# Kernel tuning notes

Hardware: AMD Instinct MI355X
Metric: run time of the kernel (lower is better)

Reference implementation:

```python
import jax, jax.numpy as jnp
import numpy as np

B, L, K, G, C, S = 1024, 32, 8, 8, 128, 32
D_IN = 2 * L + K + S  # masked z (L) + mask (L) + target (K) + shared (S)
TAU = 1.0
EPS = 1e-5
NEG_INF = -1e9  # stands in for torch's -9e15 diagonal fill; sigmoid(-1e9)=0


def setup_inputs() -> dict:
    key = jax.random.key(0)
    ks = jax.random.split(key, 24)
    eye = jnp.eye(K, dtype=bool)
    kaiming = lambda k, shape: jax.random.uniform(k, shape, jnp.float32, -1.0, 1.0) * np.sqrt(6.0 / shape[-1])
    return {
        "z_sample": jax.random.normal(ks[0], (B, L), jnp.float32),
        "target": jax.random.randint(ks[1], (B,), 0, K),
        "z_mean": jax.random.normal(ks[2], (B, L), jnp.float32),
        "z_logstd": 0.1 * jax.random.normal(ks[3], (B, L), jnp.float32),
        "z_shared": jax.random.normal(ks[4], (B, S), jnp.float32),
        "u_gumbel": jax.random.uniform(ks[5], (B, L, K), jnp.float32),
        "u_adj": jax.random.uniform(ks[6], (B, G, K, K), jnp.float32),
        "target_params": 0.1 * jax.random.normal(ks[7], (L, K), jnp.float32),
        "enco_theta": jnp.where(eye, NEG_INF, jax.random.normal(ks[8], (K, K), jnp.float32)),
        "enco_gamma": jnp.where(eye, NEG_INF, jax.random.normal(ks[9], (K, K), jnp.float32)),
        "W1": kaiming(ks[10], (L, C, D_IN)),
        "b1": jnp.zeros((L, C), jnp.float32),
        "gn1_w": jnp.ones((L, C), jnp.float32),
        "gn1_b": jnp.zeros((L, C), jnp.float32),
        "W2": kaiming(ks[11], (L, C, C)),
        "b2": jnp.zeros((L, C), jnp.float32),
        "gn2_w": jnp.ones((L, C), jnp.float32),
        "gn2_b": jnp.zeros((L, C), jnp.float32),
        "W3": 0.01 * jax.random.normal(ks[12], (L, 2, C), jnp.float32),
        "b3": jnp.zeros((L, 2), jnp.float32),
        "tanh_scale": jnp.zeros((L, 2), jnp.float32),
    }


def _mv_linear(x, W, b):
    # x: [B,G,L,d_in], W: [L,d_out,d_in] -> [B,G,L,d_out]  (per-latent independent linear)
    return jnp.einsum("bgld,lhd->bglh", x, W) + b


def _mv_groupnorm(x, w, b):
    # GroupNorm(L groups over L*C channels) == per-(sample, latent) normalization over C
    mu = x.mean(-1, keepdims=True)
    var = ((x - mu) ** 2).mean(-1, keepdims=True)
    return (x - mu) * jax.lax.rsqrt(var + EPS) * w + b


def reference(z_sample, target, z_mean, z_logstd, z_shared, u_gumbel, u_adj,
              target_params, enco_theta, enco_gamma,
              W1, b1, gn1_w, gn1_b, W2, b2, gn2_w, gn2_b, W3, b3, tanh_scale):
    dt = z_sample.dtype
    target_oh = jax.nn.one_hot(target, K, dtype=dt)  # [B,K]

    # hard gumbel-softmax with straight-through estimator: psi assigns latents to causal vars
    g = -jnp.log(-jnp.log(u_gumbel + 1e-10) + 1e-10)
    soft = jax.nn.softmax((target_params[None] + g) / TAU, axis=-1)  # [B,L,K]
    hard = jax.nn.one_hot(jnp.argmax(soft, axis=-1), K, dtype=dt)
    psi = hard + soft - jax.lax.stop_gradient(soft)  # [B,L,K]

    # ENCO graph sampling: edge prob = sigmoid(theta)*sigmoid(gamma), Bernoulli samples
    edge_prob = jax.nn.sigmoid(enco_theta) * jax.nn.sigmoid(enco_gamma)  # [K,K]
    adj = (u_adj < edge_prob[None, None]).astype(dt)  # [B,G,K,K], adj[k,l]=1: k->l

    # latent-level parent mask: mask[b,g,i,j]=1 iff latent j is a parent of latent i
    latent_mask = jnp.einsum("bil,bgkl,bjk->bgij", psi, adj, psi)  # [B,G,L,L]
    latent_mask = latent_mask * (1.0 - jnp.eye(L, dtype=dt))

    # per-latent network input: [masked parents, mask, intervention indicator, shared]
    z_masked = latent_mask * z_sample[:, None, None, :]                        # [B,G,L,L]
    t_inp = jnp.broadcast_to((psi * target_oh[:, None, :])[:, None], (B, G, L, K))
    zs = jnp.broadcast_to(z_shared[:, None, None, :], (B, G, L, S))
    s_inp = jnp.concatenate([z_masked, latent_mask, t_inp, zs], axis=-1)       # [B,G,L,D_IN]

    h = jax.nn.silu(_mv_groupnorm(_mv_linear(s_inp, W1, b1), gn1_w, gn1_b))
    h = jax.nn.silu(_mv_groupnorm(_mv_linear(h, W2, b2), gn2_w, gn2_b))
    h = _mv_linear(h, W3, b3)                                                  # [B,G,L,2]
    sc = jnp.exp(tanh_scale)                                                   # [L,2]
    h = jnp.tanh(h / sc) * sc                                                  # MultivarStableTanh
    prior_mean, prior_logstd = h[..., 0], h[..., 1]                            # [B,G,L]

    # KL(q(z) || p(z)) per latent, averaged over graph samples, summed over latents
    var_q = jnp.exp(2.0 * z_logstd)[:, None]                                   # [B,1,L]
    kld = (prior_logstd - z_logstd[:, None]
           + (var_q + (z_mean[:, None] - prior_mean) ** 2) / (2.0 * jnp.exp(2.0 * prior_logstd))
           - 0.5)                                                              # [B,G,L]
    return kld.mean(axis=1).sum(axis=-1)                                       # [B]
```

## Files before the change

kernel.cpp:

```cpp
#include <hip/hip_runtime.h>
#include <hip/hip_bf16.h>

#define B_DIM 1024
#define L_DIM 32
#define K_DIM 8
#define G_DIM 8
#define C_DIM 128
#define S_DIM 32
#define DIN   104

typedef __bf16  bf16x8 __attribute__((ext_vector_type(8)));
typedef float   f32x4  __attribute__((ext_vector_type(4)));

union frag_u { uint4 u; bf16x8 v; };

static __device__ __forceinline__ unsigned int pk2(float a, float b) {
    __hip_bfloat162 h = __float22bfloat162_rn(make_float2(a, b));
    union { __hip_bfloat162 h; unsigned int u; } v; v.h = h; return v.u;
}
static __device__ __forceinline__ bf16x8 ld_frag(const unsigned short* p) {
    frag_u t; t.u = *(const uint4*)p; return t.v;
}
static __device__ __forceinline__ bf16x8 u2f(uint4 u) {
    frag_u t; t.u = u; return t.v;
}
static __device__ __forceinline__ float siluf(float x) {
    return __fdividef(x, 1.0f + __expf(-x));
}

__global__ __launch_bounds__(256) void prep_kernel(
    const float* __restrict__ u_gumbel,
    const float* __restrict__ u_adj,
    const float* __restrict__ target_params,
    const float* __restrict__ enco_theta,
    const float* __restrict__ enco_gamma,
    const int*   __restrict__ target,
    const float* __restrict__ W1,
    const float* __restrict__ W2,
    float*       __restrict__ out,
    unsigned char* __restrict__ cvarpk,
    unsigned int*  __restrict__ wsmask,
    unsigned short* __restrict__ wscr)
{
    const int t = threadIdx.x;
    if (blockIdx.x >= 1024) {
        int gtid  = (blockIdx.x - 1024) * 256 + t;
        int lane  = gtid & 63;
        int ks    = (gtid >> 6) & 3;
        int mt    = (gtid >> 8) & 3;
        int wm    = (gtid >> 10) & 1;
        int l     = (gtid >> 11) & 31;
        int which = gtid >> 16;
        int m  = 16 * (4 * wm + mt) + (lane & 15);
        int k0 = ks * 32 + (lane >> 4) * 8;
        uint4 o;
        if (which == 0) {
            if (k0 >= 104) {
                o = make_uint4(0u, 0u, 0u, 0u);
            } else {
                const float* p = W1 + (size_t)l * 13312 + m * 104 + k0;
                float4 a = *(const float4*)p, bq = *(const float4*)(p + 4);
                o = make_uint4(pk2(a.x, a.y), pk2(a.z, a.w), pk2(bq.x, bq.y), pk2(bq.z, bq.w));
            }
        } else {
            const float* p = W2 + (size_t)l * 16384 + m * 128 + k0;
            float4 a = *(const float4*)p, bq = *(const float4*)(p + 4);
            o = make_uint4(pk2(a.x, a.y), pk2(a.z, a.w), pk2(bq.x, bq.y), pk2(bq.z, bq.w));
        }
        *(uint4*)(wscr + (size_t)gtid * 8) = o;
        return;
    }

    __shared__ double ep[64];
    __shared__ unsigned char cv8[32];
    __shared__ unsigned long long adjb[8];
    const int b = blockIdx.x;
    if (t < 64) {
        double th = (double)enco_theta[t];
        double ga = (double)enco_gamma[t];
        ep[t] = (1.0 / (1.0 + exp(-th))) * (1.0 / (1.0 + exp(-ga)));
    }
    if (t == 0) out[b] = 0.0f;
    __syncthreads();

    {
        const int l = t >> 3, k = t & 7;
        float uf = u_gumbel[b * 256 + t];
        float gf = -__logf(-__logf(uf + 1e-10f) + 1e-10f);
        float vf = target_params[t] + gf;
        float vm = vf; int bk = k;
        #pragma unroll
        for (int off = 1; off < 8; off <<= 1) {
            float ov = __shfl_xor(vm, off, 64);
            int  obk = __shfl_xor(bk, off, 64);
            if (ov > vm || (ov == vm && obk < bk)) { vm = ov; bk = obk; }
        }
        int amb = ((k != bk) && (vm - vf < 1e-3f)) ? 1 : 0;
        #pragma unroll
        for (int off = 1; off < 8; off <<= 1) amb |= __shfl_xor(amb, off, 64);
        if (amb) {
            double ud = (double)uf;
            double gd = -log(-log(ud + 1e-10) + 1e-10);
            double vd = (double)target_params[t] + gd;
            int bk2 = k;
            #pragma unroll
            for (int off = 1; off < 8; off <<= 1) {
                double ov = __shfl_xor(vd, off, 64);
                int   obk = __shfl_xor(bk2, off, 64);
                if (ov > vd || (ov == vd && obk < bk2)) { vd = ov; bk2 = obk; }
            }
            bk = bk2;
        }
        if (k == 0) {
            int tg = target[b];
            unsigned char pkd = (unsigned char)(bk | ((bk == tg) ? 8 : 0));
            cvarpk[b * 32 + l] = pkd;
            cv8[l] = pkd;
        }
    }
    {
        const int wv = t >> 6, lane = t & 63;
        #pragma unroll
        for (int q = 0; q < 2; ++q) {
            int gg = wv + 4 * q;
            double u = (double)u_adj[b * 512 + gg * 64 + lane];
            unsigned long long m = __ballot(u < ep[lane]);
            if (lane == 0) adjb[gg] = m;
        }
    }
    __syncthreads();

    {
        const int g = t >> 5, l = t & 31;
        int lam = cv8[l] & 7;
        unsigned long long bits = adjb[g] >> lam;
        unsigned int mask = 0u;
        #pragma unroll
        for (int j = 0; j < 32; ++j) {
            int kap = cv8[j] & 7;
            mask |= ((unsigned int)(bits >> (kap * 8)) & 1u) << j;
        }
        mask &= ~(1u << l);
        wsmask[l * 8192 + b * 8 + g] = mask;
    }
}

__global__ __launch_bounds__(256, 3) void fused_kernel(
    const float* __restrict__ z_sample,
    const float* __restrict__ z_mean,
    const float* __restrict__ z_logstd,
    const float* __restrict__ z_shared,
    const float* __restrict__ pb1,
    const float* __restrict__ g1w,
    const float* __restrict__ g1b,
    const float* __restrict__ pb2,
    const float* __restrict__ g2w,
    const float* __restrict__ g2b,
    const float* __restrict__ W3,
    const float* __restrict__ pb3,
    const float* __restrict__ tsc,
    const unsigned short* __restrict__ wscr,
    const unsigned char*  __restrict__ cvarpk,
    const unsigned int*   __restrict__ wsmask,
    float* __restrict__ out)
{
    __shared__ __align__(16) unsigned short XH[4][32][136];
    __shared__ float p_g1w[128], p_g1b[128], p_b1[128];
    __shared__ float p_g2w[128], p_g2b[128], p_b2[128];
    __shared__ float p_w3[2][128];
    __shared__ float p_b3[2], p_ts[2];
    __shared__ unsigned int  msk[128];
    __shared__ unsigned char cvl[16];

    const int tid  = threadIdx.x;
    const int w    = tid >> 6, lane = tid & 63;
    const int lo   = lane & 15, hi = lane >> 4;
    const int l    = blockIdx.x & 31;
    const int grp  = blockIdx.x >> 5;

    if (tid < 128) {
        int c = tid;
        p_g1w[c] = g1w[l * 128 + c];  p_g1b[c] = g1b[l * 128 + c];
        p_b1[c]  = pb1[l * 128 + c];  p_w3[0][c] = W3[l * 256 + c];
        msk[c]   = wsmask[l * 8192 + grp * 128 + c];
    } else {
        int c = tid - 128;
        p_g2w[c] = g2w[l * 128 + c];  p_g2b[c] = g2b[l * 128 + c];
        p_b2[c]  = pb2[l * 128 + c];  p_w3[1][c] = W3[l * 256 + 128 + c];
    }
    if (tid < 16) cvl[tid] = cvarpk[(size_t)(grp * 16 + tid) * 32 + l];
    if (tid == 0) {
        p_b3[0] = pb3[l * 2];  p_b3[1] = pb3[l * 2 + 1];
        p_ts[0] = tsc[l * 2];  p_ts[1] = tsc[l * 2 + 1];
    }
    __syncthreads();

    bf16x8 bq[2][4];
    #pragma unroll
    for (int nt = 0; nt < 2; ++nt) {
        int r  = w * 32 + nt * 16 + lo;
        int bl = r >> 3;
        int bg = grp * 16 + bl;
        unsigned int m32 = msk[r];
        unsigned int mq  = (m32 >> (hi * 8)) & 0xffu;
        const float4* zp = (const float4*)(z_sample + bg * 32 + hi * 8);
        float4 za = zp[0], zb = zp[1];
        uint4 f0;
        f0.x = pk2((mq & 1u)   ? za.x : 0.f, (mq & 2u)   ? za.y : 0.f);
        f0.y = pk2((mq & 4u)   ? za.z : 0.f, (mq & 8u)   ? za.w : 0.f);
        f0.z = pk2((mq & 16u)  ? zb.x : 0.f, (mq & 32u)  ? zb.y : 0.f);
        f0.w = pk2((mq & 64u)  ? zb.z : 0.f, (mq & 128u) ? zb.w : 0.f);
        uint4 f1;
        f1.x = ((mq & 1u)   ? 0x3F80u : 0u) | ((mq & 2u)   ? 0x3F800000u : 0u);
        f1.y = ((mq & 4u)   ? 0x3F80u : 0u) | ((mq & 8u)   ? 0x3F800000u : 0u);
        f1.z = ((mq & 16u)  ? 0x3F80u : 0u) | ((mq & 32u)  ? 0x3F800000u : 0u);
        f1.w = ((mq & 64u)  ? 0x3F80u : 0u) | ((mq & 128u) ? 0x3F800000u : 0u);
        unsigned int cb8 = cvl[bl];
        int lam = cb8 & 7, tf = (cb8 >> 3) & 1;
        int zsb = (hi == 0) ? 24 : (hi - 1) * 8;
        const float4* sp = (const float4*)(z_shared + bg * 32 + zsb);
        float4 sa = sp[0], sb = sp[1];
        uint4 fz;
        fz.x = pk2(sa.x, sa.y); fz.y = pk2(sa.z, sa.w);
        fz.z = pk2(sb.x, sb.y); fz.w = pk2(sb.z, sb.w);
        unsigned int ohw = tf ? (0x3F80u << ((lam & 1) << 4)) : 0u;
        int lq = lam >> 1;
        uint4 fo;
        fo.x = (lq == 0) ? ohw : 0u;
        fo.y = (lq == 1) ? ohw : 0u;
        fo.z = (lq == 2) ? ohw : 0u;
        fo.w = (lq == 3) ? ohw : 0u;
        bool h0 = (hi == 0);
        uint4 f2, f3;
        f2.x = h0 ? fo.x : fz.x;  f2.y = h0 ? fo.y : fz.y;
        f2.z = h0 ? fo.z : fz.z;  f2.w = h0 ? fo.w : fz.w;
        f3.x = h0 ? fz.x : 0u;    f3.y = h0 ? fz.y : 0u;
        f3.z = h0 ? fz.z : 0u;    f3.w = h0 ? fz.w : 0u;
        bq[nt][0] = u2f(f0); bq[nt][1] = u2f(f1);
        bq[nt][2] = u2f(f2); bq[nt][3] = u2f(f3);
    }

    const float inv128 = 1.0f / 128.0f;

    f32x4 acc[8][2];
    #pragma unroll
    for (int cb = 0; cb < 8; ++cb)
        #pragma unroll
        for (int nt = 0; nt < 2; ++nt) acc[cb][nt] = (f32x4){0.f, 0.f, 0.f, 0.f};
    {
        const unsigned short* w1p = wscr + (size_t)(l * 32) * 512 + lane * 8;
        #pragma unroll
        for (int ks = 0; ks < 4; ++ks) {
            #pragma unroll
            for (int half = 0; half < 2; ++half) {
                bf16x8 wf[4];
                #pragma unroll
                for (int q = 0; q < 4; ++q)
                    wf[q] = ld_frag(w1p + ((half * 4 + q) * 4 + ks) * 512);
                #pragma unroll
                for (int q = 0; q < 4; ++q) {
                    int cb = half * 4 + q;
                    acc[cb][0] = __builtin_amdgcn_mfma_f32_16x16x32_bf16(
                        wf[q], bq[0][ks], acc[cb][0], 0, 0, 0);
                    acc[cb][1] = __builtin_amdgcn_mfma_f32_16x16x32_bf16(
                        wf[q], bq[1][ks], acc[cb][1], 0, 0, 0);
                }
            }
        }
    }

    float s1[2] = {0.f, 0.f}, s2[2] = {0.f, 0.f};
    #pragma unroll
    for (int cb = 0; cb < 8; ++cb) {
        float4 b4 = *(const float4*)&p_b1[cb * 16 + hi * 4];
        #pragma unroll
        for (int rg = 0; rg < 4; ++rg) {
            float bias = ((const float*)&b4)[rg];
            #pragma unroll
            for (int nt = 0; nt < 2; ++nt) {
                float v = acc[cb][nt][rg] + bias;
                acc[cb][nt][rg] = v;
                s1[nt] += v;  s2[nt] += v * v;
            }
        }
    }
    float mu[2], rstd[2];
    #pragma unroll
    for (int nt = 0; nt < 2; ++nt) {
        s1[nt] += __shfl_xor(s1[nt], 16, 64);  s1[nt] += __shfl_xor(s1[nt], 32, 64);
        s2[nt] += __shfl_xor(s2[nt], 16, 64);  s2[nt] += __shfl_xor(s2[nt], 32, 64);
        float m_  = s1[nt] * inv128;
        float var = s2[nt] * inv128 - m_ * m_;
        mu[nt] = m_;  rstd[nt] = rsqrtf(var + 1e-5f);
    }
    #pragma unroll
    for (int cb = 0; cb < 8; ++cb) {
        float4 gw4 = *(const float4*)&p_g1w[cb * 16 + hi * 4];
        float4 gb4 = *(const float4*)&p_g1b[cb * 16 + hi * 4];
        #pragma unroll
        for (int nt = 0; nt < 2; ++nt) {
            float sl[4];
            #pragma unroll
            for (int rg = 0; rg < 4; ++rg) {
                float x = (acc[cb][nt][rg] - mu[nt]) * rstd[nt] * ((const float*)&gw4)[rg]
                          + ((const float*)&gb4)[rg];
                sl[rg] = siluf(x);
            }
            *(uint2*)&XH[w][nt * 16 + lo][cb * 16 + hi * 4] =
                make_uint2(pk2(sl[0], sl[1]), pk2(sl[2], sl[3]));
        }
    }

    #pragma unroll
    for (int cb = 0; cb < 8; ++cb)
        #pragma unroll
        for (int nt = 0; nt < 2; ++nt) acc[cb][nt] = (f32x4){0.f, 0.f, 0.f, 0.f};
    {
        const unsigned short* w2p = wscr + (size_t)((32 + l) * 32) * 512 + lane * 8;
        #pragma unroll
        for (int ks = 0; ks < 4; ++ks) {
            bf16x8 bf0 = ld_frag(&XH[w][lo][ks * 32 + hi * 8]);
            bf16x8 bf1 = ld_frag(&XH[w][16 + lo][ks * 32 + hi * 8]);
            #pragma unroll
            for (int half = 0; half < 2; ++half) {
                bf16x8 wf[4];
                #pragma unroll
                for (int q = 0; q < 4; ++q)
                    wf[q] = ld_frag(w2p + ((half * 4 + q) * 4 + ks) * 512);
                #pragma unroll
                for (int q = 0; q < 4; ++q) {
                    int cb = half * 4 + q;
                    acc[cb][0] = __builtin_amdgcn_mfma_f32_16x16x32_bf16(
                        wf[q], bf0, acc[cb][0], 0, 0, 0);
                    acc[cb][1] = __builtin_amdgcn_mfma_f32_16x16x32_bf16(
                        wf[q], bf1, acc[cb][1], 0, 0, 0);
                }
            }
        }
    }

    float t1[2] = {0.f, 0.f}, t2[2] = {0.f, 0.f};
    #pragma unroll
    for (int cb = 0; cb < 8; ++cb) {
        float4 b4 = *(const float4*)&p_b2[cb * 16 + hi * 4];
        #pragma unroll
        for (int rg = 0; rg < 4; ++rg) {
            float bias = ((const float*)&b4)[rg];
            #pragma unroll
            for (int nt = 0; nt < 2; ++nt) {
                float v = acc[cb][nt][rg] + bias;
                acc[cb][nt][rg] = v;
                t1[nt] += v;  t2[nt] += v * v;
            }
        }
    }
    float mu2[2], rstd2[2];
    #pragma unroll
    for (int nt = 0; nt < 2; ++nt) {
        t1[nt] += __shfl_xor(t1[nt], 16, 64);  t1[nt] += __shfl_xor(t1[nt], 32, 64);
        t2[nt] += __shfl_xor(t2[nt], 16, 64);  t2[nt] += __shfl_xor(t2[nt], 32, 64);
        float m_  = t1[nt] * inv128;
        float var = t2[nt] * inv128 - m_ * m_;
        mu2[nt] = m_;  rstd2[nt] = rsqrtf(var + 1e-5f);
    }
    float pmp[2] = {0.f, 0.f}, plp[2] = {0.f, 0.f};
    #pragma unroll
    for (int cb = 0; cb < 8; ++cb) {
        float4 gw4 = *(const float4*)&p_g2w[cb * 16 + hi * 4];
        float4 gb4 = *(const float4*)&p_g2b[cb * 16 + hi * 4];
        float4 w04 = *(const float4*)&p_w3[0][cb * 16 + hi * 4];
        float4 w14 = *(const float4*)&p_w3[1][cb * 16 + hi * 4];
        #pragma unroll
        for (int rg = 0; rg < 4; ++rg) {
            float wg = ((const float*)&gw4)[rg], gb = ((const float*)&gb4)[rg];
            float w0 = ((const float*)&w04)[rg], w1 = ((const float*)&w14)[rg];
            #pragma unroll
            for (int nt = 0; nt < 2; ++nt) {
                float x  = (acc[cb][nt][rg] - mu2[nt]) * rstd2[nt] * wg + gb;
                float sl = siluf(x);
                pmp[nt] += sl * w0;
                plp[nt] += sl * w1;
            }
        }
    }
    #pragma unroll
    for (int nt = 0; nt < 2; ++nt) {
        pmp[nt] += __shfl_xor(pmp[nt], 16, 64);  pmp[nt] += __shfl_xor(pmp[nt], 32, 64);
        plp[nt] += __shfl_xor(plp[nt], 16, 64);  plp[nt] += __shfl_xor(plp[nt], 32, 64);
    }

    {
        float sc0 = __expf(p_ts[0]), sc1 = __expf(p_ts[1]);
        float is0 = __expf(-p_ts[0]), is1 = __expf(-p_ts[1]);
        #pragma unroll
        for (int nt = 0; nt < 2; ++nt) {
            float pm = pmp[nt] + p_b3[0];
            float pl = plp[nt] + p_b3[1];
            float e0 = __expf(2.0f * pm * is0);
            pm = (1.0f - 2.0f * __fdividef(1.0f, e0 + 1.0f)) * sc0;
            float e1 = __expf(2.0f * pl * is1);
            pl = (1.0f - 2.0f * __fdividef(1.0f, e1 + 1.0f)) * sc1;
            int r  = w * 32 + nt * 16 + lo;
            int bg = grp * 16 + (r >> 3);
            float zm = z_mean[bg * 32 + l];
            float zl = z_logstd[bg * 32 + l];
            float vq = __expf(2.0f * zl);
            float d  = zm - pm;
            float kld = pl - zl + (vq + d * d) * 0.5f * __expf(-2.0f * pl) - 0.5f;
            kld += __shfl_xor(kld, 1, 64);
            kld += __shfl_xor(kld, 2, 64);
            kld += __shfl_xor(kld, 4, 64);
            if (hi == 0 && (lo & 7) == 0) atomicAdd(&out[bg], kld * 0.125f);
        }
    }
}

extern "C" void kernel_launch(void* const* d_in, const int* in_sizes, int n_in,
                              void* d_out, int out_size, void* d_ws, size_t ws_size,
                              hipStream_t stream) {
    const float* z_sample      = (const float*)d_in[0];
    const int*   target        = (const int*)d_in[1];
    const float* z_mean        = (const float*)d_in[2];
    const float* z_logstd      = (const float*)d_in[3];
    const float* z_shared      = (const float*)d_in[4];
    const float* u_gumbel      = (const float*)d_in[5];
    const float* u_adj         = (const float*)d_in[6];
    const float* target_params = (const float*)d_in[7];
    const float* enco_theta    = (const float*)d_in[8];
    const float* enco_gamma    = (const float*)d_in[9];
    const float* W1            = (const float*)d_in[10];
    const float* pb1           = (const float*)d_in[11];
    const float* g1w           = (const float*)d_in[12];
    const float* g1b           = (const float*)d_in[13];
    const float* W2            = (const float*)d_in[14];
    const float* pb2           = (const float*)d_in[15];
    const float* g2w           = (const float*)d_in[16];
    const float* g2b           = (const float*)d_in[17];
    const float* W3            = (const float*)d_in[18];
    const float* pb3           = (const float*)d_in[19];
    const float* tsc           = (const float*)d_in[20];

    unsigned char* cvarpk = (unsigned char*)d_ws;
    unsigned int*  wsmask = (unsigned int*)((char*)d_ws + 32768);
    unsigned short* wscr  = (unsigned short*)((char*)d_ws + 32768 + 1048576);

    prep_kernel<<<1536, 256, 0, stream>>>(u_gumbel, u_adj, target_params,
                                          enco_theta, enco_gamma, target,
                                          W1, W2, (float*)d_out,
                                          cvarpk, wsmask, wscr);
    fused_kernel<<<2048, 256, 0, stream>>>(z_sample, z_mean, z_logstd, z_shared,
                                           pb1, g1w, g1b, pb2, g2w, g2b,
                                           W3, pb3, tsc, wscr, cvarpk, wsmask,
                                           (float*)d_out);
}
```

Baseline: 169.8 us.

## Cut register pressure: stage layer-1 inputs in LDS, double-buffer weight fragments

The layer-1 B-operand fragments are written to the per-wave XH shared buffer instead of being held in 32 registers. Both GEMM loops now prefetch the next pair of weight fragments while issuing four MFMAs on the current pair. The launch-bounds minimum-blocks hint rises from 3 to 4. GroupNorm is folded into one multiply-add per element with a precomputed offset. The goal is higher occupancy and better load/MFMA overlap, at the cost of extra LDS traffic and a tighter register budget that could cause spills.

```diff
diff --git a/kernel.cpp b/kernel.cpp
--- a/kernel.cpp
+++ b/kernel.cpp
@@ -20,9 +20,6 @@
 }
 static __device__ __forceinline__ bf16x8 ld_frag(const unsigned short* p) {
     frag_u t; t.u = *(const uint4*)p; return t.v;
-}
-static __device__ __forceinline__ bf16x8 u2f(uint4 u) {
-    frag_u t; t.u = u; return t.v;
 }
 static __device__ __forceinline__ float siluf(float x) {
     return __fdividef(x, 1.0f + __expf(-x));
@@ -145,7 +142,7 @@
     }
 }
 
-__global__ __launch_bounds__(256, 3) void fused_kernel(
+__global__ __launch_bounds__(256, 4) void fused_kernel(
     const float* __restrict__ z_sample,
     const float* __restrict__ z_mean,
     const float* __restrict__ z_logstd,
@@ -195,13 +192,12 @@
     }
     __syncthreads();
 
-    bf16x8 bq[2][4];
     #pragma unroll
     for (int nt = 0; nt < 2; ++nt) {
-        int r  = w * 32 + nt * 16 + lo;
-        int bl = r >> 3;
+        int r  = nt * 16 + lo;
+        int bl = (w * 32 + r) >> 3;
         int bg = grp * 16 + bl;
-        unsigned int m32 = msk[r];
+        unsigned int m32 = msk[w * 32 + r];
         unsigned int mq  = (m32 >> (hi * 8)) & 0xffu;
         const float4* zp = (const float4*)(z_sample + bg * 32 + hi * 8);
         float4 za = zp[0], zb = zp[1];
@@ -236,11 +232,15 @@
         f2.z = h0 ? fo.z : fz.z;  f2.w = h0 ? fo.w : fz.w;
         f3.x = h0 ? fz.x : 0u;    f3.y = h0 ? fz.y : 0u;
         f3.z = h0 ? fz.z : 0u;    f3.w = h0 ? fz.w : 0u;
-        bq[nt][0] = u2f(f0); bq[nt][1] = u2f(f1);
-        bq[nt][2] = u2f(f2); bq[nt][3] = u2f(f3);
+        *(uint4*)&XH[w][r][hi * 8]      = f0;
+        *(uint4*)&XH[w][r][32 + hi * 8] = f1;
+        *(uint4*)&XH[w][r][64 + hi * 8] = f2;
+        *(uint4*)&XH[w][r][96 + hi * 8] = f3;
     }
 
     const float inv128 = 1.0f / 128.0f;
+    const unsigned short* w1p = wscr + (size_t)(l * 32) * 512 + lane * 8;
+    const unsigned short* w2p = wscr + (size_t)((32 + l) * 32) * 512 + lane * 8;
 
     f32x4 acc[8][2];
     #pragma unroll
@@ -248,23 +248,27 @@
         #pragma unroll
         for (int nt = 0; nt < 2; ++nt) acc[cb][nt] = (f32x4){0.f, 0.f, 0.f, 0.f};
     {
-        const unsigned short* w1p = wscr + (size_t)(l * 32) * 512 + lane * 8;
+        bf16x8 wfA[2], wfB[2];
+        wfA[0] = ld_frag(w1p + 0 * 512);
+        wfA[1] = ld_frag(w1p + 4 * 512);
         #pragma unroll
         for (int ks = 0; ks < 4; ++ks) {
-            #pragma unroll
-            for (int half = 0; half < 2; ++half) {
-                bf16x8 wf[4];
-                #pragma unroll
-                for (int q = 0; q < 4; ++q)
-                    wf[q] = ld_frag(w1p + ((half * 4 + q) * 4 + ks) * 512);
-                #pragma unroll
-                for (int q = 0; q < 4; ++q) {
-                    int cb = half * 4 + q;
-                    acc[cb][0] = __builtin_amdgcn_mfma_f32_16x16x32_bf16(
-                        wf[q], bq[0][ks], acc[cb][0], 0, 0, 0);
-                    acc[cb][1] = __builtin_amdgcn_mfma_f32_16x16x32_bf16(
-                        wf[q], bq[1][ks], acc[cb][1], 0, 0, 0);
+            bf16x8 bf0 = ld_frag(&XH[w][lo][ks * 32 + hi * 8]);
+            bf16x8 bf1 = ld_frag(&XH[w][16 + lo][ks * 32 + hi * 8]);
+            #pragma unroll
+            for (int p = 0; p < 4; ++p) {
+                int ncb = (p < 3) ? (2 * p + 2) : 0;
+                int nks = (p < 3) ? ks : ks + 1;
+                if (p < 3 || ks < 3) {
+                    wfB[0] = ld_frag(w1p + (ncb * 4 + nks) * 512);
+                    wfB[1] = ld_frag(w1p + ((ncb + 1) * 4 + nks) * 512);
                 }
+                int cb = 2 * p;
+                acc[cb][0]     = __builtin_amdgcn_mfma_f32_16x16x32_bf16(wfA[0], bf0, acc[cb][0], 0, 0, 0);
+                acc[cb][1]     = __builtin_amdgcn_mfma_f32_16x16x32_bf16(wfA[0], bf1, acc[cb][1], 0, 0, 0);
+                acc[cb + 1][0] = __builtin_amdgcn_mfma_f32_16x16x32_bf16(wfA[1], bf0, acc[cb + 1][0], 0, 0, 0);
+                acc[cb + 1][1] = __builtin_amdgcn_mfma_f32_16x16x32_bf16(wfA[1], bf1, acc[cb + 1][1], 0, 0, 0);
+                wfA[0] = wfB[0];  wfA[1] = wfB[1];
             }
         }
     }
@@ -284,14 +288,15 @@
             }
         }
     }
-    float mu[2], rstd[2];
+    float rstd[2], nrm_off[2];
     #pragma unroll
     for (int nt = 0; nt < 2; ++nt) {
         s1[nt] += __shfl_xor(s1[nt], 16, 64);  s1[nt] += __shfl_xor(s1[nt], 32, 64);
         s2[nt] += __shfl_xor(s2[nt], 16, 64);  s2[nt] += __shfl_xor(s2[nt], 32, 64);
         float m_  = s1[nt] * inv128;
         float var = s2[nt] * inv128 - m_ * m_;
-        mu[nt] = m_;  rstd[nt] = rsqrtf(var + 1e-5f);
+        float r   = rsqrtf(var + 1e-5f);
+        rstd[nt] = r;  nrm_off[nt] = -m_ * r;
     }
     #pragma unroll
     for (int cb = 0; cb < 8; ++cb) {
@@ -302,8 +307,8 @@
             float sl[4];
             #pragma unroll
             for (int rg = 0; rg < 4; ++rg) {
-                float x = (acc[cb][nt][rg] - mu[nt]) * rstd[nt] * ((const float*)&gw4)[rg]
-                          + ((const float*)&gb4)[rg];
+                float tn = acc[cb][nt][rg] * rstd[nt] + nrm_off[nt];
+                float x  = tn * ((const float*)&gw4)[rg] + ((const float*)&gb4)[rg];
                 sl[rg] = siluf(x);
             }
             *(uint2*)&XH[w][nt * 16 + lo][cb * 16 + hi * 4] =
@@ -316,25 +321,27 @@
         #pragma unroll
         for (int nt = 0; nt < 2; ++nt) acc[cb][nt] = (f32x4){0.f, 0.f, 0.f, 0.f};
     {
-        const unsigned short* w2p = wscr + (size_t)((32 + l) * 32) * 512 + lane * 8;
+        bf16x8 wfA[2], wfB[2];
+        wfA[0] = ld_frag(w2p + 0 * 512);
+        wfA[1] = ld_frag(w2p + 4 * 512);
         #pragma unroll
         for (int ks = 0; ks < 4; ++ks) {
             bf16x8 bf0 = ld_frag(&XH[w][lo][ks * 32 + hi * 8]);
             bf16x8 bf1 = ld_frag(&XH[w][16 + lo][ks * 32 + hi * 8]);
             #pragma unroll
-            for (int half = 0; half < 2; ++half) {
-                bf16x8 wf[4];
-                #pragma unroll
-                for (int q = 0; q < 4; ++q)
-                    wf[q] = ld_frag(w2p + ((half * 4 + q) * 4 + ks) * 512);
-                #pragma unroll
-                for (int q = 0; q < 4; ++q) {
-                    int cb = half * 4 + q;
-                    acc[cb][0] = __builtin_amdgcn_mfma_f32_16x16x32_bf16(
-                        wf[q], bf0, acc[cb][0], 0, 0, 0);
-                    acc[cb][1] = __builtin_amdgcn_mfma_f32_16x16x32_bf16(
-                        wf[q], bf1, acc[cb][1], 0, 0, 0);
+            for (int p = 0; p < 4; ++p) {
+                int ncb = (p < 3) ? (2 * p + 2) : 0;
+                int nks = (p < 3) ? ks : ks + 1;
+                if (p < 3 || ks < 3) {
+                    wfB[0] = ld_frag(w2p + (ncb * 4 + nks) * 512);
+                    wfB[1] = ld_frag(w2p + ((ncb + 1) * 4 + nks) * 512);
                 }
+                int cb = 2 * p;
+                acc[cb][0]     = __builtin_amdgcn_mfma_f32_16x16x32_bf16(wfA[0], bf0, acc[cb][0], 0, 0, 0);
+                acc[cb][1]     = __builtin_amdgcn_mfma_f32_16x16x32_bf16(wfA[0], bf1, acc[cb][1], 0, 0, 0);
+                acc[cb + 1][0] = __builtin_amdgcn_mfma_f32_16x16x32_bf16(wfA[1], bf0, acc[cb + 1][0], 0, 0, 0);
+                acc[cb + 1][1] = __builtin_amdgcn_mfma_f32_16x16x32_bf16(wfA[1], bf1, acc[cb + 1][1], 0, 0, 0);
+                wfA[0] = wfB[0];  wfA[1] = wfB[1];
             }
         }
     }
@@ -354,14 +361,15 @@
             }
         }
     }
-    float mu2[2], rstd2[2];
+    float rstd2[2], off2[2];
     #pragma unroll
     for (int nt = 0; nt < 2; ++nt) {
         t1[nt] += __shfl_xor(t1[nt], 16, 64);  t1[nt] += __shfl_xor(t1[nt], 32, 64);
         t2[nt] += __shfl_xor(t2[nt], 16, 64);  t2[nt] += __shfl_xor(t2[nt], 32, 64);
         float m_  = t1[nt] * inv128;
         float var = t2[nt] * inv128 - m_ * m_;
-        mu2[nt] = m_;  rstd2[nt] = rsqrtf(var + 1e-5f);
+        float r   = rsqrtf(var + 1e-5f);
+        rstd2[nt] = r;  off2[nt] = -m_ * r;
     }
     float pmp[2] = {0.f, 0.f}, plp[2] = {0.f, 0.f};
     #pragma unroll
@@ -376,7 +384,8 @@
             float w0 = ((const float*)&w04)[rg], w1 = ((const float*)&w14)[rg];
             #pragma unroll
             for (int nt = 0; nt < 2; ++nt) {
-                float x  = (acc[cb][nt][rg] - mu2[nt]) * rstd2[nt] * wg + gb;
+                float tn = acc[cb][nt][rg] * rstd2[nt] + off2[nt];
+                float x  = tn * wg + gb;
                 float sl = siluf(x);
                 pmp[nt] += sl * w0;
                 plp[nt] += sl * w1;
```

After: 167.5 us. No clear change (-1.4%).
